# Kernel optimization log

Hardware: AMD Instinct MI355X
Metric: run time of the kernel (lower is better)

Reference implementation:

```python
import jax, jax.numpy as jnp
import numpy as np

D_MODEL = 1024
NUM_HEADS = 16
D_HEAD = D_MODEL // NUM_HEADS


def setup_inputs() -> dict:
    key = jax.random.key(0)
    ks = jax.random.split(key, 8)
    B, S = 2, 2048
    query_x = jax.random.normal(ks[0], (B, S, D_MODEL), dtype=jnp.float32)
    key_x = jax.random.normal(ks[1], (B, S, D_MODEL), dtype=jnp.float32)
    value_x = jax.random.normal(ks[2], (B, S, D_MODEL), dtype=jnp.float32)
    mask = jnp.zeros((S, S), dtype=jnp.float32)  # additive mask, broadcast over B,H
    scale = np.sqrt(2.0 / D_MODEL)  # kaiming-ish init
    w_query = jax.random.normal(ks[3], (D_MODEL, D_MODEL), dtype=jnp.float32) * scale
    w_key = jax.random.normal(ks[4], (D_MODEL, D_MODEL), dtype=jnp.float32) * scale
    w_value = jax.random.normal(ks[5], (D_MODEL, D_MODEL), dtype=jnp.float32) * scale
    w0 = jax.random.normal(ks[6], (D_MODEL, D_MODEL), dtype=jnp.float32) * scale
    return {"query_x": query_x, "key_x": key_x, "value_x": value_x, "mask": mask,
            "w_query": w_query, "w_key": w_key, "w_value": w_value, "w0": w0}


def reference(query_x, key_x, value_x, mask, w_query, w_key, w_value, w0):
    B, S, _ = query_x.shape
    # nn.Linear applies x @ W.T; weights stored [out, in]
    def proj(x, w):
        y = jnp.einsum('bsd,ed->bse', x, w)              # [B,S,D]
        return y.reshape(B, S, NUM_HEADS, D_HEAD).transpose(0, 2, 1, 3)  # [B,H,S,Dh]
    q = proj(query_x, w_query)
    k = proj(key_x, w_key)
    v = proj(value_x, w_value)
    scores = jnp.einsum('bhqd,bhkd->bhqk', q, k) / jnp.sqrt(jnp.float32(D_HEAD))
    scores = scores + mask  # broadcast additive mask
    attn = jax.nn.softmax(scores, axis=-1)
    out = jnp.einsum('bhqk,bhkd->bhqd', attn, v)         # [B,H,S,Dh]
    out = out.transpose(0, 2, 1, 3).reshape(B, S, NUM_HEADS * D_HEAD)
    return jnp.einsum('bsd,ed->bse', out, w0)
```

## Files before the change

### kernel.cpp

```cpp
#include <hip/hip_runtime.h>
#include <hip/hip_bf16.h>
#include <stdint.h>

#define D_MODEL 1024
#define NH 16
#define DH 64
#define SEQ 2048
#define MROWS 4096
#define LOG2E 1.44269504088896340736f

typedef unsigned short ushort_t;
typedef __attribute__((ext_vector_type(4))) float f32x4;
typedef __attribute__((ext_vector_type(16))) float f32x16;
typedef __attribute__((ext_vector_type(4))) unsigned short us4;
typedef __attribute__((ext_vector_type(8))) unsigned short us8;
typedef __attribute__((ext_vector_type(4))) unsigned int u32x4;
typedef __attribute__((ext_vector_type(8))) __bf16 bf16x8;

__device__ __forceinline__ f32x4 mfma16(us8 a, us8 b, f32x4 c) {
    return __builtin_amdgcn_mfma_f32_16x16x32_bf16(
        __builtin_bit_cast(bf16x8, a), __builtin_bit_cast(bf16x8, b), c, 0, 0, 0);
}
__device__ __forceinline__ f32x16 mfma32(us8 a, us8 b, f32x16 c) {
    return __builtin_amdgcn_mfma_f32_32x32x16_bf16(
        __builtin_bit_cast(bf16x8, a), __builtin_bit_cast(bf16x8, b), c, 0, 0, 0);
}

__device__ __forceinline__ unsigned int cvtpk(float lo, float hi) {
    unsigned int r;
    asm("v_cvt_pk_bf16_f32 %0, %1, %2" : "=v"(r) : "v"(lo), "v"(hi));
    return r;
}
__device__ __forceinline__ ushort_t f2bf1(float f) {
    return (ushort_t)(cvtpk(f, f) & 0xffffu);
}

__device__ __forceinline__ float exp2_fast(float x) {
#if __has_builtin(__builtin_amdgcn_exp2f)
    return __builtin_amdgcn_exp2f(x);
#else
    float r; asm("v_exp_f32 %0, %1" : "=v"(r) : "v"(x)); return r;
#endif
}

__device__ __forceinline__ void gload16(const void* g, void* l) {
    __builtin_amdgcn_global_load_lds(
        (const __attribute__((address_space(1))) void*)g,
        (__attribute__((address_space(3))) void*)l, 16, 0, 0);
}

__global__ __launch_bounds__(256) void conv_multi(
    const float* __restrict__ s0, ushort_t* __restrict__ d0,
    const float* __restrict__ s1, ushort_t* __restrict__ d1,
    const float* __restrict__ s2, ushort_t* __restrict__ d2,
    const float* __restrict__ s3, ushort_t* __restrict__ d3, int n4)
{
    int z = blockIdx.z;
    const float* s = z == 0 ? s0 : z == 1 ? s1 : z == 2 ? s2 : s3;
    ushort_t* d    = z == 0 ? d0 : z == 1 ? d1 : z == 2 ? d2 : d3;
    int i = blockIdx.x * 256 + threadIdx.x;
    int stride = gridDim.x * 256;
    for (; i < n4; i += stride) {
        float4 v = ((const float4*)s)[i];
        uint2 pr;
        pr.x = cvtpk(v.x, v.y);
        pr.y = cvtpk(v.z, v.w);
        ((uint2*)d)[i] = pr;
    }
}

__global__ __launch_bounds__(256) void mask_flags(const float* __restrict__ mask,
                                                  int* __restrict__ flags)
{
    int qt = blockIdx.x, kt = blockIdx.y;
    int t = threadIdx.x;
    bool nz = false;
#pragma unroll
    for (int i = 0; i < 4; i++) {
        int idx = t + i * 256;
        int row = idx >> 4, c4 = (idx & 15) * 4;
        float4 v = *(const float4*)(mask + (size_t)(qt * 64 + row) * SEQ + kt * 64 + c4);
        nz |= (v.x != 0.f) | (v.y != 0.f) | (v.z != 0.f) | (v.w != 0.f);
    }
    if (__any((int)nz) && (t & 63) == 0) atomicOr(&flags[qt * 32 + kt], 1);
}

__device__ __forceinline__ void stageB_bf16(const ushort_t* __restrict__ B,
                                            int n0, int t, int w, int k0,
                                            ushort_t* sB)
{
#pragma unroll
    for (int r = 0; r < 2; r++) {
        int chunk = r * 256 + t;
        int row = chunk >> 3, cc = (chunk & 7) ^ (row & 7);
        gload16(B + (size_t)(n0 + row) * D_MODEL + k0 + cc * 8,
                &sB[(r * 256 + w * 64) * 8]);
    }
}

__device__ __forceinline__ void stageA_bf16(const ushort_t* __restrict__ A,
                                            int m0, int t, int w, int k0,
                                            ushort_t* sA)
{
#pragma unroll
    for (int r = 0; r < 4; r++) {
        int chunk = r * 256 + t;
        int row = chunk >> 3, cc = (chunk & 7) ^ (row & 7);
        gload16(A + (size_t)(m0 + row) * D_MODEL + k0 + cc * 8,
                &sA[(r * 256 + w * 64) * 8]);
    }
}

__device__ __forceinline__ void stageA_f32(const float* __restrict__ A,
                                           int m0, int t, int k0,
                                           ushort_t* sA)
{
#pragma unroll
    for (int r = 0; r < 4; r++) {
        int chunk = r * 256 + t;
        int row = chunk >> 3, c = chunk & 7;
        const float* src = A + (size_t)(m0 + row) * D_MODEL + k0 + c * 8;
        float4 v0 = *(const float4*)src;
        float4 v1 = *(const float4*)(src + 4);
        u32x4 pw;
        pw[0] = cvtpk(v0.x, v0.y); pw[1] = cvtpk(v0.z, v0.w);
        pw[2] = cvtpk(v1.x, v1.y); pw[3] = cvtpk(v1.z, v1.w);
        int by = (row * 128 + c * 16) ^ ((row & 7) << 4);
        *(u32x4*)((char*)sA + by) = pw;
    }
}

__global__ __launch_bounds__(256) void gemm_qkv(const ushort_t* __restrict__ Aq,
                                                const ushort_t* __restrict__ Ak,
                                                const ushort_t* __restrict__ Av,
                                                const float* __restrict__ vx,
                                                const ushort_t* __restrict__ Wq,
                                                const ushort_t* __restrict__ Wk,
                                                const ushort_t* __restrict__ Wv,
                                                ushort_t* __restrict__ Qo,
                                                ushort_t* __restrict__ Ko,
                                                ushort_t* __restrict__ VT)
{
    __shared__ ushort_t sA[2][128 * 64];
    __shared__ ushort_t sB[2][64 * 64];
    const int z = blockIdx.z;
    const ushort_t* Abf = z == 0 ? Aq : z == 1 ? Ak : Av;
    const ushort_t* W = z == 0 ? Wq : z == 1 ? Wk : Wv;
    const bool f32path = (z == 2) && (Av == nullptr);
    const int t = threadIdx.x, lane = t & 63, w = t >> 6;
    const int lr = lane & 15, lg = lane >> 4;
    const int wm = (w >> 1) * 64, wn = (w & 1) * 32;
    const int m0 = blockIdx.x * 128, n0 = blockIdx.y * 64;

    f32x4 acc[4][2];
    f32x4 zero = {0.f, 0.f, 0.f, 0.f};
#pragma unroll
    for (int i = 0; i < 4; i++)
#pragma unroll
        for (int j = 0; j < 2; j++) acc[i][j] = zero;

    stageB_bf16(W, n0, t, w, 0, &sB[0][0]);
    if (!f32path) stageA_bf16(Abf, m0, t, w, 0, &sA[0][0]);
    else          stageA_f32(vx, m0, t, 0, &sA[0][0]);
    __syncthreads();

    for (int it = 0; it < D_MODEL / 64; ++it) {
        const int cur = it & 1;
        const char* cA = (const char*)&sA[cur][0];
        const char* cB = (const char*)&sB[cur][0];
        const bool more = (it + 1 < D_MODEL / 64);

        us8 af[4][2], bfr[2][2];
#pragma unroll
        for (int i = 0; i < 4; i++)
#pragma unroll
            for (int ks = 0; ks < 2; ks++) {
                int row = wm + i * 16 + lr;
                af[i][ks] = *(const us8*)(cA + ((row * 128 + (ks * 32 + 8 * lg) * 2)
                                                ^ ((row & 7) << 4)));
            }
#pragma unroll
        for (int j = 0; j < 2; j++)
#pragma unroll
            for (int ks = 0; ks < 2; ks++) {
                int row = wn + j * 16 + lr;
                bfr[j][ks] = *(const us8*)(cB + ((row * 128 + (ks * 32 + 8 * lg) * 2)
                                                 ^ ((row & 7) << 4)));
            }

        if (more) {
            stageB_bf16(W, n0, t, w, (it + 1) * 64, &sB[cur ^ 1][0]);
            if (!f32path) stageA_bf16(Abf, m0, t, w, (it + 1) * 64, &sA[cur ^ 1][0]);
            else          stageA_f32(vx, m0, t, (it + 1) * 64, &sA[cur ^ 1][0]);
        }

#pragma unroll
        for (int i = 0; i < 4; i++)
#pragma unroll
            for (int j = 0; j < 2; j++)
#pragma unroll
                for (int ks = 0; ks < 2; ks++)
                    acc[i][j] = mfma16(af[i][ks], bfr[j][ks], acc[i][j]);

        __syncthreads();
    }

    if (z < 2) {
        ushort_t* C = z ? Ko : Qo;
        const float scale = z ? 1.0f : 0.125f * LOG2E;
#pragma unroll
        for (int i = 0; i < 4; i++)
#pragma unroll
            for (int j = 0; j < 2; j++)
#pragma unroll
                for (int r = 0; r < 4; r++) {
                    int m = m0 + wm + i * 16 + 4 * lg + r;
                    int n = n0 + wn + j * 16 + lr;
                    int b = m >> 11, s = m & 2047;
                    int h = n >> 6, dh = n & 63;
                    C[(((size_t)(b * NH + h)) * SEQ + s) * DH + dh] = f2bf1(acc[i][j][r] * scale);
                }
    } else {
#pragma unroll
        for (int i = 0; i < 4; i++)
#pragma unroll
            for (int j = 0; j < 2; j++) {
                int m = m0 + wm + i * 16 + 4 * lg;
                int n = n0 + wn + j * 16 + lr;
                int b = m >> 11, s = m & 2047;
                int h = n >> 6, dh = n & 63;
                uint2 pr;
                pr.x = cvtpk(acc[i][j][0], acc[i][j][1]);
                pr.y = cvtpk(acc[i][j][2], acc[i][j][3]);
                *(uint2*)&VT[(((size_t)(b * NH + h)) * DH + dh) * SEQ + s] = pr;
            }
    }
}

__global__ __launch_bounds__(256) void gemm_o(const ushort_t* __restrict__ A,
                                              const ushort_t* __restrict__ W,
                                              float* __restrict__ C)
{
    __shared__ ushort_t sA[2][128 * 64];
    __shared__ ushort_t sB[2][64 * 64];
    const int t = threadIdx.x, lane = t & 63, w = t >> 6;
    const int lr = lane & 15, lg = lane >> 4;
    const int wm = (w >> 1) * 64, wn = (w & 1) * 32;
    const int m0 = blockIdx.x * 128, n0 = blockIdx.y * 64;

    f32x4 acc[4][2];
    f32x4 zero = {0.f, 0.f, 0.f, 0.f};
#pragma unroll
    for (int i = 0; i < 4; i++)
#pragma unroll
        for (int j = 0; j < 2; j++) acc[i][j] = zero;

    stageA_bf16(A, m0, t, w, 0, &sA[0][0]);
    stageB_bf16(W, n0, t, w, 0, &sB[0][0]);
    __syncthreads();

    for (int it = 0; it < D_MODEL / 64; ++it) {
        const int cur = it & 1;
        const char* cA = (const char*)&sA[cur][0];
        const char* cB = (const char*)&sB[cur][0];

        us8 af[4][2], bfr[2][2];
#pragma unroll
        for (int i = 0; i < 4; i++)
#pragma unroll
            for (int ks = 0; ks < 2; ks++) {
                int row = wm + i * 16 + lr;
                af[i][ks] = *(const us8*)(cA + ((row * 128 + (ks * 32 + 8 * lg) * 2)
                                                ^ ((row & 7) << 4)));
            }
#pragma unroll
        for (int j = 0; j < 2; j++)
#pragma unroll
            for (int ks = 0; ks < 2; ks++) {
                int row = wn + j * 16 + lr;
                bfr[j][ks] = *(const us8*)(cB + ((row * 128 + (ks * 32 + 8 * lg) * 2)
                                                 ^ ((row & 7) << 4)));
            }

        if (it + 1 < D_MODEL / 64) {
            stageA_bf16(A, m0, t, w, (it + 1) * 64, &sA[cur ^ 1][0]);
            stageB_bf16(W, n0, t, w, (it + 1) * 64, &sB[cur ^ 1][0]);
        }

#pragma unroll
        for (int i = 0; i < 4; i++)
#pragma unroll
            for (int j = 0; j < 2; j++)
#pragma unroll
                for (int ks = 0; ks < 2; ks++)
                    acc[i][j] = mfma16(af[i][ks], bfr[j][ks], acc[i][j]);

        __syncthreads();
    }

#pragma unroll
    for (int i = 0; i < 4; i++)
#pragma unroll
        for (int j = 0; j < 2; j++)
#pragma unroll
            for (int r = 0; r < 4; r++) {
                int m = m0 + wm + i * 16 + 4 * lg + r;
                int n = n0 + wn + j * 16 + lr;
                C[(size_t)m * D_MODEL + n] = acc[i][j][r];
            }
}

__global__ __launch_bounds__(256, 2) void attn_fwd(const ushort_t* __restrict__ Q,
                                                   const ushort_t* __restrict__ K,
                                                   const ushort_t* __restrict__ VT,
                                                   const float* __restrict__ mask,
                                                   const int* __restrict__ flags,
                                                   ushort_t* __restrict__ O)
{
    __shared__ ushort_t sK[2][64 * 64];
    __shared__ ushort_t sVT[2][64 * 64];

    const int t = threadIdx.x, lane = t & 63, w = t >> 6;
    const int l31 = lane & 31, lh = lane >> 5;
    const int id = blockIdx.x;
    const int bh = (id & 7) * 4 + ((id >> 3) >> 4);
    const int qt = (id >> 3) & 15;
    const int b = bh >> 4, h = bh & 15;
    const int q = qt * 128 + w * 32 + l31;

    unsigned long long blt = __ballot(flags[(qt * 2 + lh) * 32 + l31] != 0);
    const unsigned int fl = (unsigned int)(blt | (blt >> 32));

    us8 qfr[4];
#pragma unroll
    for (int ks = 0; ks < 4; ks++)
        qfr[ks] = *(const us8*)(Q + ((size_t)bh * SEQ + q) * DH + ks * 16 + 8 * lh);

    f32x16 acc_o[2];
#pragma unroll
    for (int d = 0; d < 2; d++)
#pragma unroll
        for (int r = 0; r < 16; r++) acc_o[d][r] = 0.f;
    float acc_l = 0.f;

    const ushort_t* Kb = K + (size_t)bh * SEQ * DH;
    const ushort_t* Vb = VT + (size_t)bh * DH * SEQ;

    const ushort_t* kp[2];
    const ushort_t* vp[2];
#pragma unroll
    for (int r = 0; r < 2; r++) {
        int j = r * 256 + t;
        int row = j >> 3, cc = (j & 7) ^ (row & 7);
        kp[r] = Kb + (size_t)row * DH + cc * 8;
        vp[r] = Vb + (size_t)row * SEQ + cc * 8;
    }

#define STAGE(kvt_, buf_)                                                     \
    {                                                                         \
        _Pragma("unroll")                                                     \
        for (int r = 0; r < 2; r++)                                           \
            gload16(kp[r] + (size_t)(kvt_) * (64 * DH),                       \
                    &sK[buf_][(r * 256 + w * 64) * 8]);                       \
        _Pragma("unroll")                                                     \
        for (int r = 0; r < 2; r++)                                           \
            gload16(vp[r] + (size_t)(kvt_) * 64,                              \
                    &sVT[buf_][(r * 256 + w * 64) * 8]);                      \
    }

    STAGE(0, 0);
    __syncthreads();

    for (int kvt = 0; kvt < SEQ / 64; ++kvt) {
        const int cur = kvt & 1;
        const char* cK = (const char*)sK[cur];
        const char* cV = (const char*)sVT[cur];

        f32x16 sacc[2];
#pragma unroll
        for (int kb = 0; kb < 2; kb++)
#pragma unroll
            for (int r = 0; r < 16; r++) sacc[kb][r] = 0.f;
        __builtin_amdgcn_s_setprio(1);
#pragma unroll
        for (int ks = 0; ks < 4; ks++)
#pragma unroll
            for (int kb = 0; kb < 2; kb++) {
                int row = kb * 32 + l31;
                int by = (row * 128 + (ks * 16 + 8 * lh) * 2) ^ ((row & 7) << 4);
                us8 kf = *(const us8*)(cK + by);
                sacc[kb] = mfma32(kf, qfr[ks], sacc[kb]);
            }
        __builtin_amdgcn_s_setprio(0);

        us8 vf[4][2];
#pragma unroll
        for (int ks = 0; ks < 4; ks++)
#pragma unroll
            for (int dblk = 0; dblk < 2; dblk++) {
                int row = dblk * 32 + l31;
                int by = (row * 128 + (ks * 16 + 8 * lh) * 2) ^ ((row & 7) << 4);
                vf[ks][dblk] = *(const us8*)(cV + by);
            }

        if (kvt + 1 < SEQ / 64) STAGE(kvt + 1, cur ^ 1);

        if ((fl >> kvt) & 1u) {
#pragma unroll
            for (int kb = 0; kb < 2; kb++)
#pragma unroll
                for (int r = 0; r < 16; r++) {
                    int kcol = kb * 32 + (r & 3) + 8 * (r >> 2) + 4 * lh;
                    sacc[kb][r] += mask[(size_t)q * SEQ + kvt * 64 + kcol] * LOG2E;
                }
        }

        float rs = 0.f;
#pragma unroll
        for (int kb = 0; kb < 2; kb++)
#pragma unroll
            for (int r = 0; r < 16; r++) {
                float p = exp2_fast(sacc[kb][r]);
                sacc[kb][r] = p;
                rs += p;
            }
        rs += __shfl_xor(rs, 32);
        acc_l += rs;

        __builtin_amdgcn_s_setprio(1);
#pragma unroll
        for (int ks = 0; ks < 4; ks++) {
            const int kb = ks >> 1, u = ks & 1;
            unsigned int W0 = cvtpk(sacc[kb][8 * u + 0], sacc[kb][8 * u + 1]);
            unsigned int W1 = cvtpk(sacc[kb][8 * u + 2], sacc[kb][8 * u + 3]);
            unsigned int W2 = cvtpk(sacc[kb][8 * u + 4], sacc[kb][8 * u + 5]);
            unsigned int W3 = cvtpk(sacc[kb][8 * u + 6], sacc[kb][8 * u + 7]);
            asm("v_permlane32_swap_b32 %0, %1" : "+v"(W0), "+v"(W2));
            asm("v_permlane32_swap_b32 %0, %1" : "+v"(W1), "+v"(W3));
            u32x4 pw;
            pw[0] = W0; pw[1] = W1; pw[2] = W2; pw[3] = W3;
            us8 pf = __builtin_bit_cast(us8, pw);
#pragma unroll
            for (int dblk = 0; dblk < 2; dblk++)
                acc_o[dblk] = mfma32(vf[ks][dblk], pf, acc_o[dblk]);
        }
        __builtin_amdgcn_s_setprio(0);

        __syncthreads();
    }

    float inv = 1.f / acc_l;
    ushort_t* Orow = O + ((size_t)(b * SEQ) + q) * D_MODEL + h * DH;
#pragma unroll
    for (int dblk = 0; dblk < 2; dblk++)
#pragma unroll
        for (int g = 0; g < 4; g++) {
            unsigned int lo = cvtpk(acc_o[dblk][4 * g + 0] * inv,
                                    acc_o[dblk][4 * g + 1] * inv);
            unsigned int hi = cvtpk(acc_o[dblk][4 * g + 2] * inv,
                                    acc_o[dblk][4 * g + 3] * inv);
            uint2 pr; pr.x = lo; pr.y = hi;
            *(uint2*)(Orow + dblk * 32 + 8 * g + 4 * lh) = pr;
        }
#undef STAGE
}

extern "C" void kernel_launch(void* const* d_in, const int* in_sizes, int n_in,
                              void* d_out, int out_size, void* d_ws, size_t ws_size,
                              hipStream_t stream)
{
    const float* qx   = (const float*)d_in[0];
    const float* kx   = (const float*)d_in[1];
    const float* vx   = (const float*)d_in[2];
    const float* mask = (const float*)d_in[3];
    const float* wq   = (const float*)d_in[4];
    const float* wk   = (const float*)d_in[5];
    const float* wv   = (const float*)d_in[6];
    const float* w0   = (const float*)d_in[7];
    float* out = (float*)d_out;

    char* ws = (char*)d_ws;
    const size_t MB = 1024 * 1024;
    ushort_t* Aq = (ushort_t*)(ws);
    ushort_t* Ak = (ushort_t*)(ws + 8 * MB);
    ushort_t* AO = (ushort_t*)(ws + 8 * MB);
    ushort_t* Wq = (ushort_t*)(ws + 16 * MB);
    ushort_t* Wk = (ushort_t*)(ws + 18 * MB);
    ushort_t* Wv = (ushort_t*)(ws + 20 * MB);
    ushort_t* W0 = (ushort_t*)(ws + 22 * MB);
    ushort_t* VT = (ushort_t*)(ws + 24 * MB);

    const bool bigws = (ws_size >= 41 * MB);
    ushort_t* Av = bigws ? (ushort_t*)(ws + 32 * MB) : nullptr;
    int* flags   = (int*)(ws + (bigws ? 40 * MB : 32 * MB));

    ushort_t* Qb = (ushort_t*)d_out;
    ushort_t* Kb = (ushort_t*)d_out + 4 * MB;

    hipMemsetAsync(flags, 0, 32 * 32 * sizeof(int), stream);
    mask_flags<<<dim3(32, 32), 256, 0, stream>>>(mask, flags);

    conv_multi<<<dim3(256, 1, 4), 256, 0, stream>>>(wq, Wq, wk, Wk, wv, Wv, w0, W0, 262144);
    conv_multi<<<dim3(1024, 1, bigws ? 3 : 2), 256, 0, stream>>>(
        qx, Aq, kx, Ak, vx, bigws ? Av : Aq, qx, Aq, 1048576);

    gemm_qkv<<<dim3(32, 16, 3), 256, 0, stream>>>(Aq, Ak, Av, vx,
                                                  Wq, Wk, Wv, Qb, Kb, VT);

    attn_fwd<<<512, 256, 0, stream>>>(Qb, Kb, VT, mask, flags, AO);

    gemm_o<<<dim3(32, 16), 256, 0, stream>>>(AO, W0, out);
}
```

Before: 125.4 us.

## Split attention KV range in two halves and combine partial outputs

Adds a templated split-KV mode to the attention kernel: each (batch, head, query-tile) is handled by two blocks that each process half of the key/value tiles. Each block writes unnormalized bf16 partial outputs and its row sums. A new combine kernel then adds the two partials and divides by the summed row sums. The aim is to double the block count for better CU utilization and load balance. In exchange it adds extra global traffic and a kernel launch for the partial buffers, and rounds the partials to bf16 before combining. The split path is used only when the workspace is large enough.

```diff
diff --git a/kernel.cpp b/kernel.cpp
--- a/kernel.cpp
+++ b/kernel.cpp
@@ -33,6 +33,10 @@
 }
 __device__ __forceinline__ ushort_t f2bf1(float f) {
     return (ushort_t)(cvtpk(f, f) & 0xffffu);
+}
+__device__ __forceinline__ float bf2f(ushort_t u) {
+    union { unsigned int u; float f; } v; v.u = ((unsigned int)u) << 16;
+    return v.f;
 }
 
 __device__ __forceinline__ float exp2_fast(float x) {
@@ -85,6 +89,27 @@
     if (__any((int)nz) && (t & 63) == 0) atomicOr(&flags[qt * 32 + kt], 1);
 }
 
+__global__ __launch_bounds__(256) void combine(const ushort_t* __restrict__ O1,
+                                               const ushort_t* __restrict__ O2,
+                                               const float* __restrict__ L1,
+                                               const float* __restrict__ L2,
+                                               ushort_t* __restrict__ AO)
+{
+    int i = blockIdx.x * 256 + threadIdx.x;
+    int base = i * 8;
+    int row = base >> 10, h = (base & 1023) >> 6;
+    float invl = 1.f / (L1[row * NH + h] + L2[row * NH + h]);
+    us8 a = *(const us8*)(O1 + base);
+    us8 c = *(const us8*)(O2 + base);
+    float f[8];
+#pragma unroll
+    for (int e = 0; e < 8; e++) f[e] = (bf2f(a[e]) + bf2f(c[e])) * invl;
+    u32x4 o;
+    o[0] = cvtpk(f[0], f[1]); o[1] = cvtpk(f[2], f[3]);
+    o[2] = cvtpk(f[4], f[5]); o[3] = cvtpk(f[6], f[7]);
+    *(u32x4*)(AO + base) = o;
+}
+
 __device__ __forceinline__ void stageB_bf16(const ushort_t* __restrict__ B,
                                             int n0, int t, int w, int k0,
                                             ushort_t* sB)
@@ -310,12 +335,17 @@
             }
 }
 
+template<bool SPLIT>
 __global__ __launch_bounds__(256, 2) void attn_fwd(const ushort_t* __restrict__ Q,
                                                    const ushort_t* __restrict__ K,
                                                    const ushort_t* __restrict__ VT,
                                                    const float* __restrict__ mask,
                                                    const int* __restrict__ flags,
-                                                   ushort_t* __restrict__ O)
+                                                   ushort_t* __restrict__ O,
+                                                   ushort_t* __restrict__ O1,
+                                                   ushort_t* __restrict__ O2,
+                                                   float* __restrict__ L1,
+                                                   float* __restrict__ L2)
 {
     __shared__ ushort_t sK[2][64 * 64];
     __shared__ ushort_t sVT[2][64 * 64];
@@ -323,10 +353,22 @@
     const int t = threadIdx.x, lane = t & 63, w = t >> 6;
     const int l31 = lane & 31, lh = lane >> 5;
     const int id = blockIdx.x;
-    const int bh = (id & 7) * 4 + ((id >> 3) >> 4);
-    const int qt = (id >> 3) & 15;
+    int bh, qt, half;
+    if (SPLIT) {
+        const int rest = id >> 3;
+        qt = rest & 15;
+        const int hh = rest >> 4;
+        bh = (id & 7) * 4 + (hh & 3);
+        half = hh >> 2;
+    } else {
+        bh = (id & 7) * 4 + ((id >> 3) >> 4);
+        qt = (id >> 3) & 15;
+        half = 0;
+    }
     const int b = bh >> 4, h = bh & 15;
     const int q = qt * 128 + w * 32 + l31;
+    const int kv0 = SPLIT ? half * 16 : 0;
+    const int nkv = SPLIT ? 16 : 32;
 
     unsigned long long blt = __ballot(flags[(qt * 2 + lh) * 32 + l31] != 0);
     const unsigned int fl = (unsigned int)(blt | (blt >> 32));
@@ -368,11 +410,12 @@
                     &sVT[buf_][(r * 256 + w * 64) * 8]);                      \
     }
 
-    STAGE(0, 0);
+    STAGE(kv0, 0);
     __syncthreads();
 
-    for (int kvt = 0; kvt < SEQ / 64; ++kvt) {
-        const int cur = kvt & 1;
+    for (int it = 0; it < nkv; ++it) {
+        const int kvt = kv0 + it;
+        const int cur = it & 1;
         const char* cK = (const char*)sK[cur];
         const char* cV = (const char*)sVT[cur];
 
@@ -403,7 +446,7 @@
                 vf[ks][dblk] = *(const us8*)(cV + by);
             }
 
-        if (kvt + 1 < SEQ / 64) STAGE(kvt + 1, cur ^ 1);
+        if (it + 1 < nkv) STAGE(kvt + 1, cur ^ 1);
 
         if ((fl >> kvt) & 1u) {
 #pragma unroll
@@ -449,19 +492,37 @@
         __syncthreads();
     }
 
-    float inv = 1.f / acc_l;
-    ushort_t* Orow = O + ((size_t)(b * SEQ) + q) * D_MODEL + h * DH;
-#pragma unroll
-    for (int dblk = 0; dblk < 2; dblk++)
-#pragma unroll
-        for (int g = 0; g < 4; g++) {
-            unsigned int lo = cvtpk(acc_o[dblk][4 * g + 0] * inv,
-                                    acc_o[dblk][4 * g + 1] * inv);
-            unsigned int hi = cvtpk(acc_o[dblk][4 * g + 2] * inv,
-                                    acc_o[dblk][4 * g + 3] * inv);
-            uint2 pr; pr.x = lo; pr.y = hi;
-            *(uint2*)(Orow + dblk * 32 + 8 * g + 4 * lh) = pr;
+    if (SPLIT) {
+        ushort_t* Op = half ? O2 : O1;
+        ushort_t* Orow = Op + ((size_t)(b * SEQ) + q) * D_MODEL + h * DH;
+#pragma unroll
+        for (int dblk = 0; dblk < 2; dblk++)
+#pragma unroll
+            for (int g = 0; g < 4; g++) {
+                unsigned int lo = cvtpk(acc_o[dblk][4 * g + 0], acc_o[dblk][4 * g + 1]);
+                unsigned int hi = cvtpk(acc_o[dblk][4 * g + 2], acc_o[dblk][4 * g + 3]);
+                uint2 pr; pr.x = lo; pr.y = hi;
+                *(uint2*)(Orow + dblk * 32 + 8 * g + 4 * lh) = pr;
+            }
+        if (lh == 0) {
+            float* Lp = half ? L2 : L1;
+            Lp[((size_t)(b * SEQ) + q) * NH + h] = acc_l;
         }
+    } else {
+        float inv = 1.f / acc_l;
+        ushort_t* Orow = O + ((size_t)(b * SEQ) + q) * D_MODEL + h * DH;
+#pragma unroll
+        for (int dblk = 0; dblk < 2; dblk++)
+#pragma unroll
+            for (int g = 0; g < 4; g++) {
+                unsigned int lo = cvtpk(acc_o[dblk][4 * g + 0] * inv,
+                                        acc_o[dblk][4 * g + 1] * inv);
+                unsigned int hi = cvtpk(acc_o[dblk][4 * g + 2] * inv,
+                                        acc_o[dblk][4 * g + 3] * inv);
+                uint2 pr; pr.x = lo; pr.y = hi;
+                *(uint2*)(Orow + dblk * 32 + 8 * g + 4 * lh) = pr;
+            }
+    }
 #undef STAGE
 }
 
@@ -481,7 +542,9 @@
 
     char* ws = (char*)d_ws;
     const size_t MB = 1024 * 1024;
+    const size_t KB = 1024;
     ushort_t* Aq = (ushort_t*)(ws);
+    ushort_t* O1p = (ushort_t*)(ws);
     ushort_t* Ak = (ushort_t*)(ws + 8 * MB);
     ushort_t* AO = (ushort_t*)(ws + 8 * MB);
     ushort_t* Wq = (ushort_t*)(ws + 16 * MB);
@@ -491,8 +554,11 @@
     ushort_t* VT = (ushort_t*)(ws + 24 * MB);
 
     const bool bigws = (ws_size >= 41 * MB);
-    ushort_t* Av = bigws ? (ushort_t*)(ws + 32 * MB) : nullptr;
-    int* flags   = (int*)(ws + (bigws ? 40 * MB : 32 * MB));
+    ushort_t* Av  = bigws ? (ushort_t*)(ws + 32 * MB) : nullptr;
+    ushort_t* O2p = (ushort_t*)(ws + 32 * MB);
+    int* flags    = (int*)(ws + (bigws ? 40 * MB : 32 * MB));
+    float* L1     = (float*)(ws + 40 * MB + 64 * KB);
+    float* L2     = (float*)(ws + 40 * MB + 384 * KB);
 
     ushort_t* Qb = (ushort_t*)d_out;
     ushort_t* Kb = (ushort_t*)d_out + 4 * MB;
@@ -507,7 +573,14 @@
     gemm_qkv<<<dim3(32, 16, 3), 256, 0, stream>>>(Aq, Ak, Av, vx,
                                                   Wq, Wk, Wv, Qb, Kb, VT);
 
-    attn_fwd<<<512, 256, 0, stream>>>(Qb, Kb, VT, mask, flags, AO);
+    if (bigws) {
+        attn_fwd<true><<<1024, 256, 0, stream>>>(Qb, Kb, VT, mask, flags,
+                                                 nullptr, O1p, O2p, L1, L2);
+        combine<<<2048, 256, 0, stream>>>(O1p, O2p, L1, L2, AO);
+    } else {
+        attn_fwd<false><<<512, 256, 0, stream>>>(Qb, Kb, VT, mask, flags,
+                                                 AO, nullptr, nullptr, nullptr, nullptr);
+    }
 
     gemm_o<<<dim3(32, 16), 256, 0, stream>>>(AO, W0, out);
 }
```

Measured after the change: 133.2 us. 6.2% more time.
